# Optimization experiments

Hardware: AMD Instinct MI355X
Metric: run time of the kernel (lower is better)

Reference implementation:

```python
import jax, jax.numpy as jnp
import numpy as np

K = 4  # number of processing steps (init kwarg)


def setup_inputs() -> dict:
    key = jax.random.key(0)
    ks = jax.random.split(key, 6)
    B, S, D = 4096, 8192, 512
    H = D  # hidden_size == input_size (residual h + f_x)
    scale = 1.0 / np.sqrt(H)
    return {
        "f_x": jax.random.normal(ks[0], (B, D), dtype=jnp.float32),
        "g_S": jax.random.normal(ks[1], (S, D), dtype=jnp.float32),
        # LSTM step: input f_x (size D), 'hidden' is concat([h, r]) of size 2H
        "W_ih": jax.random.uniform(ks[2], (4 * H, D), jnp.float32, -scale, scale),
        "W_hh": jax.random.uniform(ks[3], (4 * H, 2 * H), jnp.float32, -scale, scale),
        "b_ih": jax.random.uniform(ks[4], (4 * H,), jnp.float32, -scale, scale),
        "b_hh": jax.random.uniform(ks[5], (4 * H,), jnp.float32, -scale, scale),
    }


def _lstm_step(x, hidden, c, W_ih, W_hh, b_ih, b_hh):
    # gates: [B, 4H]; PyTorch LSTMCell gate order (i, f, g, o)
    gates = x @ W_ih.T + b_ih + hidden @ W_hh.T + b_hh
    i, f, g, o = jnp.split(gates, 4, axis=1)
    c_new = jax.nn.sigmoid(f) * c + jax.nn.sigmoid(i) * jnp.tanh(g)
    h_new = jax.nn.sigmoid(o) * jnp.tanh(c_new)
    return h_new, c_new


def reference(f_x, g_S, W_ih, W_hh, b_ih, b_hh):
    # f_x: [B, D] queries; g_S: [S, D] support set embeddings
    h = f_x
    c = jnp.zeros_like(f_x)
    for _ in range(K):
        a = jax.nn.softmax(h @ g_S.T, axis=1)       # [B, S] attention over support
        r = a @ g_S                                  # [B, D] attention readout
        concat = jnp.concatenate([h, r], axis=1)     # [B, 2D]
        h, c = _lstm_step(f_x, concat, c, W_ih, W_hh, b_ih, b_hh)
        h = h + f_x                                  # residual skip connection
    return h
```

## Files before the change

### kernel.cpp

```cpp
#include <hip/hip_runtime.h>

typedef _Float16 f16x8 __attribute__((ext_vector_type(8)));
typedef _Float16 f16x4 __attribute__((ext_vector_type(4)));
typedef float f32x4 __attribute__((ext_vector_type(4)));

#define S_DIM 8192
#define D_DIM 512

__device__ __forceinline__ void gload_lds16(const _Float16* g, _Float16* l) {
  __builtin_amdgcn_global_load_lds(
      (const __attribute__((address_space(1))) unsigned int*)g,
      (__attribute__((address_space(3))) unsigned int*)l, 16, 0, 0);
}

__device__ __forceinline__ float sigf(float x) { return 1.0f / (1.0f + __expf(-x)); }
__device__ __forceinline__ float tanhfast(float x) {
  return 1.0f - 2.0f / (__expf(2.0f * x) + 1.0f);
}


template <int BM, int BN>
__global__ __launch_bounds__(256) void gemm_bt(const _Float16* __restrict__ A, int lda,
                                               const _Float16* __restrict__ B, int ldb,
                                               _Float16* __restrict__ C, int ldc, int K) {
  constexpr int BK = 64;
  constexpr int FM = BM / 32, FN = BN / 32;
  __shared__ _Float16 As[BM * BK];
  __shared__ _Float16 Bs[BN * BK];
  const int tid = threadIdx.x;
  const int lane = tid & 63;
  const int wv = tid >> 6;
  const int bm = blockIdx.y * BM;
  const int bn = blockIdx.x * BN;
  const int wm = (wv >> 1) * (BM / 2);
  const int wn = (wv & 1) * (BN / 2);
  const int fr = lane & 15;
  const int hi4 = lane >> 4;
  const int rx7 = fr & 7;
  const int srow = lane >> 3;
  const int schk = (lane & 7) ^ srow;

  f32x4 acc[FM][FN] = {};

  for (int kt = 0; kt < K; kt += BK) {
    __syncthreads();
#pragma unroll
    for (int p = 0; p < BM / 32; ++p) {
      const int m = wv + 4 * p;
      gload_lds16(A + (size_t)(bm + 8 * m + srow) * lda + kt + schk * 8, As + 512 * m);
    }
#pragma unroll
    for (int p = 0; p < BN / 32; ++p) {
      const int m = wv + 4 * p;
      gload_lds16(B + (size_t)(bn + 8 * m + srow) * ldb + kt + schk * 8, Bs + 512 * m);
    }
    __syncthreads();

#pragma unroll
    for (int h = 0; h < 2; ++h) {
      const int co = (((h << 2) | hi4) ^ rx7) << 3;
      f16x8 af[FM], bf[FN];
#pragma unroll
      for (int i = 0; i < FM; ++i)
        af[i] = *(const f16x8*)&As[(wm + i * 16 + fr) * 64 + co];
#pragma unroll
      for (int j = 0; j < FN; ++j)
        bf[j] = *(const f16x8*)&Bs[(wn + j * 16 + fr) * 64 + co];
#pragma unroll
      for (int i = 0; i < FM; ++i)
#pragma unroll
        for (int j = 0; j < FN; ++j)
          acc[i][j] = __builtin_amdgcn_mfma_f32_16x16x32_f16(af[i], bf[j], acc[i][j], 0, 0, 0);
    }
  }

  const int cc = lane & 15;
  const int cr = (lane >> 4) * 4;
#pragma unroll
  for (int i = 0; i < FM; ++i)
#pragma unroll
    for (int j = 0; j < FN; ++j) {
      size_t base = (size_t)(bm + wm + i * 16 + cr) * ldc + (bn + wn + j * 16 + cc);
#pragma unroll
      for (int r = 0; r < 4; ++r) C[base + (size_t)r * ldc] = (_Float16)acc[i][j][r];
    }
}

__global__ __launch_bounds__(256) void gemm_rsplit(const _Float16* __restrict__ A,
                                                   const _Float16* __restrict__ B,
                                                   float* __restrict__ Ppart) {
  constexpr int BK = 64;
  __shared__ _Float16 As[128 * BK];
  __shared__ _Float16 Bs[64 * BK];
  const int tid = threadIdx.x;
  const int lane = tid & 63;
  const int wv = tid >> 6;
  const int bm = blockIdx.x * 128;
  const int bn = blockIdx.y * 64;
  const int kc = blockIdx.z;
  const int k0 = kc * 1024;
  const int wm = (wv >> 1) * 64;
  const int wn = (wv & 1) * 32;
  const int fr = lane & 15;
  const int hi4 = lane >> 4;
  const int rx7 = fr & 7;
  const int srow = lane >> 3;
  const int schk = (lane & 7) ^ srow;

  f32x4 acc[4][2] = {};

  for (int kt = k0; kt < k0 + 1024; kt += BK) {
    __syncthreads();
#pragma unroll
    for (int p = 0; p < 4; ++p) {
      const int m = wv + 4 * p;
      gload_lds16(A + (size_t)(bm + 8 * m + srow) * 16384 + kt + schk * 8, As + 512 * m);
    }
#pragma unroll
    for (int p = 0; p < 2; ++p) {
      const int m = wv + 4 * p;
      gload_lds16(B + (size_t)(bn + 8 * m + srow) * 8192 + kt + schk * 8, Bs + 512 * m);
    }
    __syncthreads();

#pragma unroll
    for (int h = 0; h < 2; ++h) {
      const int co = (((h << 2) | hi4) ^ rx7) << 3;
      f16x8 af[4], bf[2];
#pragma unroll
      for (int i = 0; i < 4; ++i)
        af[i] = *(const f16x8*)&As[(wm + i * 16 + fr) * 64 + co];
#pragma unroll
      for (int j = 0; j < 2; ++j)
        bf[j] = *(const f16x8*)&Bs[(wn + j * 16 + fr) * 64 + co];
#pragma unroll
      for (int i = 0; i < 4; ++i)
#pragma unroll
        for (int j = 0; j < 2; ++j)
          acc[i][j] = __builtin_amdgcn_mfma_f32_16x16x32_f16(af[i], bf[j], acc[i][j], 0, 0, 0);
    }
  }

  const int cc = lane & 15;
  const int cr = (lane >> 4) * 4;
#pragma unroll
  for (int i = 0; i < 4; ++i)
#pragma unroll
    for (int j = 0; j < 2; ++j) {
      size_t base = (size_t)(bm + wm + i * 16 + cr) * 8192 + 4096 + (size_t)kc * 512 +
                    (bn + wn + j * 16 + cc);
#pragma unroll
      for (int r = 0; r < 4; ++r) Ppart[base + (size_t)r * 8192] = acc[i][j][r];
    }
}

__global__ __launch_bounds__(256) void reduce_r(const float* __restrict__ Ppart,
                                                _Float16* __restrict__ rout) {
  int idx = blockIdx.x * 256 + threadIdx.x;
  int m = idx >> 7;
  int n4 = (idx & 127) * 4;
  const float* base = Ppart + (size_t)m * 8192 + 4096 + n4;
  f32x4 s = {0.f, 0.f, 0.f, 0.f};
#pragma unroll
  for (int kc = 0; kc < 8; ++kc) s += *(const f32x4*)(base + kc * 512);
  f16x4 h = {(_Float16)s[0], (_Float16)s[1], (_Float16)s[2], (_Float16)s[3]};
  *(f16x4*)&rout[(size_t)m * 512 + n4] = h;
}

__global__ __launch_bounds__(256) void gemm_scores(const _Float16* __restrict__ Ah, int ldah,
                                                   const _Float16* __restrict__ Al,
                                                   const _Float16* __restrict__ Bh,
                                                   float* __restrict__ C) {
  constexpr int BK = 64;
  __shared__ _Float16 AsH[128 * BK];
  __shared__ _Float16 AsL[128 * BK];
  __shared__ _Float16 BsH[128 * BK];
  const int tid = threadIdx.x;
  const int lane = tid & 63;
  const int wv = tid >> 6;
  const int bm = blockIdx.y * 128;
  const int bn = blockIdx.x * 128;
  const int wm = (wv >> 1) * 64;
  const int wn = (wv & 1) * 64;
  const int fr = lane & 15;
  const int hi4 = lane >> 4;
  const int rx7 = fr & 7;
  const int srow = lane >> 3;
  const int schk = (lane & 7) ^ srow;

  f32x4 acc[4][4] = {};

  for (int kt = 0; kt < 512; kt += BK) {
    __syncthreads();
#pragma unroll
    for (int p = 0; p < 4; ++p) {
      const int m = wv + 4 * p;
      const int row = 8 * m + srow;
      gload_lds16(Ah + (size_t)(bm + row) * ldah + kt + schk * 8, AsH + 512 * m);
      gload_lds16(Al + (size_t)(bm + row) * 512 + kt + schk * 8, AsL + 512 * m);
      gload_lds16(Bh + (size_t)(bn + row) * 512 + kt + schk * 8, BsH + 512 * m);
    }
    __syncthreads();

#pragma unroll
    for (int h = 0; h < 2; ++h) {
      const int co = (((h << 2) | hi4) ^ rx7) << 3;
      f16x8 fah[4], fal[4], fbh[4];
#pragma unroll
      for (int i = 0; i < 4; ++i) {
        fah[i] = *(const f16x8*)&AsH[(wm + i * 16 + fr) * 64 + co];
        fal[i] = *(const f16x8*)&AsL[(wm + i * 16 + fr) * 64 + co];
        fbh[i] = *(const f16x8*)&BsH[(wn + i * 16 + fr) * 64 + co];
      }
#pragma unroll
      for (int i = 0; i < 4; ++i)
#pragma unroll
        for (int j = 0; j < 4; ++j) {
          acc[i][j] = __builtin_amdgcn_mfma_f32_16x16x32_f16(fah[i], fbh[j], acc[i][j], 0, 0, 0);
          acc[i][j] = __builtin_amdgcn_mfma_f32_16x16x32_f16(fal[i], fbh[j], acc[i][j], 0, 0, 0);
        }
    }
  }

  const int cc = lane & 15;
  const int cr = (lane >> 4) * 4;
#pragma unroll
  for (int i = 0; i < 4; ++i)
#pragma unroll
    for (int j = 0; j < 4; ++j) {
      size_t base = (size_t)(bm + wm + i * 16 + cr) * 8192 + (bn + wn + j * 16 + cc);
#pragma unroll
      for (int r = 0; r < 4; ++r) C[base + (size_t)r * 8192] = acc[i][j][r];
    }
}

__global__ __launch_bounds__(256) void gemm_gates(const _Float16* __restrict__ Ah,
                                                  const _Float16* __restrict__ Ar,
                                                  const _Float16* __restrict__ B,
                                                  const _Float16* __restrict__ gbase,
                                                  const float* __restrict__ bsum,
                                                  const float* __restrict__ f_x,
                                                  float* __restrict__ c,
                                                  _Float16* __restrict__ hnext,
                                                  _Float16* __restrict__ h_lo,
                                                  float* __restrict__ hout) {
  __shared__ _Float16 As[128 * 64];
  __shared__ _Float16 Bs[128 * 64];
  const int tid = threadIdx.x;
  const int lane = tid & 63;
  const int wv = tid >> 6;
  const int n0 = blockIdx.x * 32;
  const int bm = blockIdx.y * 128;
  const int fr = lane & 15;
  const int hi4 = lane >> 4;
  const int rx7 = fr & 7;
  const int srow = lane >> 3;
  const int schk = (lane & 7) ^ srow;

  f32x4 acc[2][8] = {};

  for (int t = 0; t < 16; ++t) {
    const int kt = t * 64;
    __syncthreads();
#pragma unroll
    for (int p = 0; p < 4; ++p) {
      const int m = wv + 4 * p;
      const int arow = bm + 8 * m + srow;
      const _Float16* asrc = (t < 8)
                                 ? Ah + (size_t)arow * 512 + kt + schk * 8
                                 : Ar + (size_t)arow * 512 + (kt - 512) + schk * 8;
      gload_lds16(asrc, As + 512 * m);
      const int brow = 8 * m + srow;
      const int wrow = ((brow >> 5) << 9) + n0 + (brow & 31);
      gload_lds16(B + (size_t)wrow * 1024 + kt + schk * 8, Bs + 512 * m);
    }
    __syncthreads();

#pragma unroll
    for (int h = 0; h < 2; ++h) {
      const int co = (((h << 2) | hi4) ^ rx7) << 3;
      f16x8 af[2], bf[8];
#pragma unroll
      for (int i = 0; i < 2; ++i)
        af[i] = *(const f16x8*)&As[(wv * 32 + i * 16 + fr) * 64 + co];
#pragma unroll
      for (int j = 0; j < 8; ++j)
        bf[j] = *(const f16x8*)&Bs[(j * 16 + fr) * 64 + co];
#pragma unroll
      for (int i = 0; i < 2; ++i)
#pragma unroll
        for (int j = 0; j < 8; ++j)
          acc[i][j] = __builtin_amdgcn_mfma_f32_16x16x32_f16(af[i], bf[j], acc[i][j], 0, 0, 0);
    }
  }

  const int cc = lane & 15;
  const int cr = (lane >> 4) * 4;
#pragma unroll
  for (int jj = 0; jj < 2; ++jj) {
    const int colq = n0 + jj * 16 + cc;
    const float bI = bsum[colq];
    const float bF = bsum[colq + 512];
    const float bG = bsum[colq + 1024];
    const float bO = bsum[colq + 1536];
#pragma unroll
    for (int i = 0; i < 2; ++i)
#pragma unroll
      for (int r = 0; r < 4; ++r) {
        const int row = bm + wv * 32 + i * 16 + cr + r;
        const size_t g0 = (size_t)row * 2048 + colq;
        const float gi = acc[i][jj][r] + (float)gbase[g0] + bI;
        const float gf = acc[i][2 + jj][r] + (float)gbase[g0 + 512] + bF;
        const float gg = acc[i][4 + jj][r] + (float)gbase[g0 + 1024] + bG;
        const float go = acc[i][6 + jj][r] + (float)gbase[g0 + 1536] + bO;
        const size_t o = (size_t)row * 512 + colq;
        const float ci = sigf(gf) * c[o] + sigf(gi) * tanhfast(gg);
        const float hi = sigf(go) * tanhfast(ci) + f_x[o];
        c[o] = ci;
        hout[o] = hi;
        const _Float16 h16 = (_Float16)hi;
        hnext[o] = h16;
        h_lo[o] = (_Float16)(hi - (float)h16);
      }
  }
}

__global__ __launch_bounds__(256) void prep_g(const float* __restrict__ g,
                                              _Float16* __restrict__ gT,
                                              _Float16* __restrict__ g_h) {
  __shared__ _Float16 tile[64][72];
  const int s0 = blockIdx.x * 64;
  const int d0 = blockIdx.y * 64;
  const int t = threadIdx.x;
  const int r = t >> 2;
  const int cq = (t & 3) * 16;
  alignas(16) _Float16 buf[16];
#pragma unroll
  for (int q = 0; q < 4; ++q) {
    f32x4 v = *(const f32x4*)&g[(size_t)(s0 + r) * D_DIM + d0 + cq + q * 4];
#pragma unroll
    for (int e = 0; e < 4; ++e) buf[q * 4 + e] = (_Float16)v[e];
  }
#pragma unroll
  for (int k = 0; k < 16; ++k) tile[r][cq + k] = buf[k];
  *(f16x8*)&g_h[(size_t)(s0 + r) * D_DIM + d0 + cq] = *(const f16x8*)&buf[0];
  *(f16x8*)&g_h[(size_t)(s0 + r) * D_DIM + d0 + cq + 8] = *(const f16x8*)&buf[8];
  __syncthreads();
  alignas(16) _Float16 ob[16];
#pragma unroll
  for (int k = 0; k < 16; ++k) ob[k] = tile[cq + k][r];
  *(f16x8*)&gT[(size_t)(d0 + r) * S_DIM + s0 + cq] = *(const f16x8*)&ob[0];
  *(f16x8*)&gT[(size_t)(d0 + r) * S_DIM + s0 + cq + 8] = *(const f16x8*)&ob[8];
}

__global__ __launch_bounds__(256) void prep_misc(const float* __restrict__ W_ih,
                                                 const float* __restrict__ W_hh,
                                                 const float* __restrict__ f_x,
                                                 const float* __restrict__ b_ih,
                                                 const float* __restrict__ b_hh,
                                                 _Float16* __restrict__ wih_h,
                                                 _Float16* __restrict__ whh_h,
                                                 _Float16* __restrict__ hbufA,
                                                 _Float16* __restrict__ h_lo,
                                                 float* __restrict__ c,
                                                 float* __restrict__ bsum) {
  const int NW1 = 2048 * 512 / 4;
  const int NW2 = 2048 * 1024 / 4;
  const int NFX = 4096 * 512 / 4;
  int idx = blockIdx.x * 256 + threadIdx.x;
  if (idx < NW1) {
    f32x4 v = ((const f32x4*)W_ih)[idx];
    f16x4 h = {(_Float16)v[0], (_Float16)v[1], (_Float16)v[2], (_Float16)v[3]};
    ((f16x4*)wih_h)[idx] = h;
  } else if (idx < NW1 + NW2) {
    int k = idx - NW1;
    f32x4 v = ((const f32x4*)W_hh)[k];
    f16x4 h = {(_Float16)v[0], (_Float16)v[1], (_Float16)v[2], (_Float16)v[3]};
    ((f16x4*)whh_h)[k] = h;
  } else if (idx < NW1 + NW2 + NFX) {
    int k = idx - NW1 - NW2;
    f32x4 v = ((const f32x4*)f_x)[k];
    f16x4 h, lo;
#pragma unroll
    for (int e = 0; e < 4; ++e) {
      h[e] = (_Float16)v[e];
      lo[e] = (_Float16)(v[e] - (float)h[e]);
    }
    ((f16x4*)hbufA)[k] = h;
    ((f16x4*)h_lo)[k] = lo;
    f32x4 z = {0.f, 0.f, 0.f, 0.f};
    ((f32x4*)c)[k] = z;
  } else if (idx < NW1 + NW2 + NFX + 512) {
    int k = idx - NW1 - NW2 - NFX;
    f32x4 bi = ((const f32x4*)b_ih)[k];
    f32x4 bh = ((const f32x4*)b_hh)[k];
    ((f32x4*)bsum)[k] = bi + bh;
  }
}

__global__ __launch_bounds__(256) void softmax_inplace(float* __restrict__ P) {
  float* p = P + (size_t)blockIdx.x * S_DIM;
  const int tid = threadIdx.x, lane = tid & 63, wave = tid >> 6;
  __shared__ float red[8];
  float x[32];
#pragma unroll
  for (int i = 0; i < 8; ++i) {
    f32x4 v = *(const f32x4*)&p[i * 1024 + tid * 4];
#pragma unroll
    for (int j = 0; j < 4; ++j) x[i * 4 + j] = v[j];
  }
  float m = -3.0e38f;
#pragma unroll
  for (int k = 0; k < 32; ++k) m = fmaxf(m, x[k]);
#pragma unroll
  for (int o = 32; o; o >>= 1) m = fmaxf(m, __shfl_xor(m, o));
  if (lane == 0) red[wave] = m;
  __syncthreads();
  m = fmaxf(fmaxf(red[0], red[1]), fmaxf(red[2], red[3]));
  float s = 0.f;
#pragma unroll
  for (int k = 0; k < 32; ++k) {
    x[k] = exp2f((x[k] - m) * 1.44269504f);
    s += x[k];
  }
#pragma unroll
  for (int o = 32; o; o >>= 1) s += __shfl_xor(s, o);
  if (lane == 0) red[4 + wave] = s;
  __syncthreads();
  s = (red[4] + red[5]) + (red[6] + red[7]);
  float inv = 1.0f / s;
  _Float16* out = (_Float16*)p;
#pragma unroll
  for (int i = 0; i < 8; ++i) {
    f16x4 v;
#pragma unroll
    for (int j = 0; j < 4; ++j) v[j] = (_Float16)(x[i * 4 + j] * inv);
    *(f16x4*)&out[i * 1024 + tid * 4] = v;
  }
}

extern "C" void kernel_launch(void* const* d_in, const int* in_sizes, int n_in,
                              void* d_out, int out_size, void* d_ws, size_t ws_size,
                              hipStream_t stream) {
  const float* f_x = (const float*)d_in[0];
  const float* g_S = (const float*)d_in[1];
  const float* W_ih = (const float*)d_in[2];
  const float* W_hh = (const float*)d_in[3];
  const float* b_ih = (const float*)d_in[4];
  const float* b_hh = (const float*)d_in[5];
  float* hout = (float*)d_out;

  char* w = (char*)d_ws;
  float* P32 = (float*)w;
  _Float16* gbase = (_Float16*)(w + 67108864);
  _Float16* hbufA = (_Float16*)(w + 83886080);
  _Float16* hbufB = (_Float16*)(w + 88080384);
  _Float16* g_h = (_Float16*)(w + 92274688);
  _Float16* rbuf = (_Float16*)(w + 100663296);
  float* bsum = (float*)(w + 104857600);
  _Float16* gT = (_Float16*)(w + 109051904);
  _Float16* wih_h = (_Float16*)(w + 117440512);
  _Float16* whh_h = (_Float16*)(w + 119537664);
  float* c = (float*)(w + 123731968);
  _Float16* h_lo = (_Float16*)(w + 132120576);

  prep_g<<<dim3(S_DIM / 64, D_DIM / 64), 256, 0, stream>>>(g_S, gT, g_h);
  prep_misc<<<5122, 256, 0, stream>>>(W_ih, W_hh, f_x, b_ih, b_hh, wih_h, whh_h,
                                      hbufA, h_lo, c, bsum);

  gemm_bt<128, 128><<<dim3(2048 / 128, 4096 / 128), 256, 0, stream>>>(
      hbufA, 512, wih_h, 512, gbase, 2048, 512);

  for (int it = 0; it < 4; ++it) {
    _Float16* hcur = (it & 1) ? hbufB : hbufA;
    _Float16* hnxt = (it & 1) ? hbufA : hbufB;
    for (int hb = 0; hb < 2; ++hb) {
      const _Float16* hhi = hcur + (size_t)hb * 2048 * 512;
      const _Float16* hlo = h_lo + (size_t)hb * 2048 * 512;
      gemm_scores<<<dim3(64, 16), 256, 0, stream>>>(hhi, 512, hlo, g_h, P32);
      softmax_inplace<<<2048, 256, 0, stream>>>(P32);
      gemm_rsplit<<<dim3(16, 8, 8), 256, 0, stream>>>((const _Float16*)P32, gT, P32);
      reduce_r<<<1024, 256, 0, stream>>>(P32, rbuf + (size_t)hb * 2048 * 512);
    }
    gemm_gates<<<dim3(16, 32), 256, 0, stream>>>(hcur, rbuf, whh_h, gbase, bsum,
                                                 f_x, c, hnxt, h_lo, hout);
  }
  (void)in_sizes; (void)n_in; (void)out_size; (void)ws_size;
}
```

Baseline: 855.7 us.

## Fuse per-tile row max into score GEMM and store scores as fp16

The score GEMM now reduces a per-row max within each 128-column tile, writes tile-relative scores (score minus tile max) as fp16, and writes the tile maxima to a small buffer. A new softmax kernel combines those tile maxima into the global row max and rescales, so it reads fp16 instead of fp32 and no longer needs a max-reduction pass. The split-K partials for the readout GEMM are also stored in fp16 in a separate buffer rather than fp32. Together this roughly halves the memory traffic for the score matrix and the partials. The cost is lost precision in the fp16 relative scores and in the fp16 partial sums.

Measured after the change: 866.6 us. No clear change (+1.3%).

```diff
diff --git a/kernel.cpp b/kernel.cpp
--- a/kernel.cpp
+++ b/kernel.cpp
@@ -88,7 +88,7 @@
 
 __global__ __launch_bounds__(256) void gemm_rsplit(const _Float16* __restrict__ A,
                                                    const _Float16* __restrict__ B,
-                                                   float* __restrict__ Ppart) {
+                                                   _Float16* __restrict__ Pp) {
   constexpr int BK = 64;
   __shared__ _Float16 As[128 * BK];
   __shared__ _Float16 Bs[64 * BK];
@@ -114,7 +114,7 @@
 #pragma unroll
     for (int p = 0; p < 4; ++p) {
       const int m = wv + 4 * p;
-      gload_lds16(A + (size_t)(bm + 8 * m + srow) * 16384 + kt + schk * 8, As + 512 * m);
+      gload_lds16(A + (size_t)(bm + 8 * m + srow) * 8192 + kt + schk * 8, As + 512 * m);
     }
 #pragma unroll
     for (int p = 0; p < 2; ++p) {
@@ -147,34 +147,41 @@
   for (int i = 0; i < 4; ++i)
 #pragma unroll
     for (int j = 0; j < 2; ++j) {
-      size_t base = (size_t)(bm + wm + i * 16 + cr) * 8192 + 4096 + (size_t)kc * 512 +
+      size_t base = (size_t)(bm + wm + i * 16 + cr) * 4096 + (size_t)kc * 512 +
                     (bn + wn + j * 16 + cc);
 #pragma unroll
-      for (int r = 0; r < 4; ++r) Ppart[base + (size_t)r * 8192] = acc[i][j][r];
-    }
-}
-
-__global__ __launch_bounds__(256) void reduce_r(const float* __restrict__ Ppart,
+      for (int r = 0; r < 4; ++r) Pp[base + (size_t)r * 4096] = (_Float16)acc[i][j][r];
+    }
+}
+
+__global__ __launch_bounds__(256) void reduce_r(const _Float16* __restrict__ Pp,
                                                 _Float16* __restrict__ rout) {
   int idx = blockIdx.x * 256 + threadIdx.x;
   int m = idx >> 7;
   int n4 = (idx & 127) * 4;
-  const float* base = Ppart + (size_t)m * 8192 + 4096 + n4;
+  const _Float16* base = Pp + (size_t)m * 4096 + n4;
   f32x4 s = {0.f, 0.f, 0.f, 0.f};
 #pragma unroll
-  for (int kc = 0; kc < 8; ++kc) s += *(const f32x4*)(base + kc * 512);
+  for (int kc = 0; kc < 8; ++kc) {
+    f16x4 v = *(const f16x4*)(base + kc * 512);
+#pragma unroll
+    for (int e = 0; e < 4; ++e) s[e] += (float)v[e];
+  }
   f16x4 h = {(_Float16)s[0], (_Float16)s[1], (_Float16)s[2], (_Float16)s[3]};
   *(f16x4*)&rout[(size_t)m * 512 + n4] = h;
 }
 
-__global__ __launch_bounds__(256) void gemm_scores(const _Float16* __restrict__ Ah, int ldah,
-                                                   const _Float16* __restrict__ Al,
-                                                   const _Float16* __restrict__ Bh,
-                                                   float* __restrict__ C) {
+__global__ __launch_bounds__(256) void gemm_scores_rel(const _Float16* __restrict__ Ah,
+                                                       int ldah,
+                                                       const _Float16* __restrict__ Al,
+                                                       const _Float16* __restrict__ Bh,
+                                                       _Float16* __restrict__ P,
+                                                       float* __restrict__ M) {
   constexpr int BK = 64;
   __shared__ _Float16 AsH[128 * BK];
   __shared__ _Float16 AsL[128 * BK];
   __shared__ _Float16 BsH[128 * BK];
+  __shared__ float rm[2][128];
   const int tid = threadIdx.x;
   const int lane = tid & 63;
   const int wv = tid >> 6;
@@ -224,14 +231,78 @@
 
   const int cc = lane & 15;
   const int cr = (lane >> 4) * 4;
+  float rmax[4][4];
 #pragma unroll
   for (int i = 0; i < 4; ++i)
 #pragma unroll
-    for (int j = 0; j < 4; ++j) {
-      size_t base = (size_t)(bm + wm + i * 16 + cr) * 8192 + (bn + wn + j * 16 + cc);
-#pragma unroll
-      for (int r = 0; r < 4; ++r) C[base + (size_t)r * 8192] = acc[i][j][r];
-    }
+    for (int r = 0; r < 4; ++r) {
+      float m0 = fmaxf(fmaxf(acc[i][0][r], acc[i][1][r]),
+                       fmaxf(acc[i][2][r], acc[i][3][r]));
+#pragma unroll
+      for (int o = 1; o < 16; o <<= 1) m0 = fmaxf(m0, __shfl_xor(m0, o));
+      rmax[i][r] = m0;
+    }
+  if (cc == 0) {
+#pragma unroll
+    for (int i = 0; i < 4; ++i)
+#pragma unroll
+      for (int r = 0; r < 4; ++r) rm[wv & 1][wm + i * 16 + cr + r] = rmax[i][r];
+  }
+  __syncthreads();
+#pragma unroll
+  for (int i = 0; i < 4; ++i)
+#pragma unroll
+    for (int r = 0; r < 4; ++r) {
+      const int row = wm + i * 16 + cr + r;
+      const float mt = fmaxf(rm[0][row], rm[1][row]);
+      if (cc == 0 && (wv & 1) == 0)
+        M[(size_t)(bm + row) * 64 + blockIdx.x] = mt;
+#pragma unroll
+      for (int j = 0; j < 4; ++j)
+        P[(size_t)(bm + row) * 8192 + bn + wn + j * 16 + cc] =
+            (_Float16)(acc[i][j][r] - mt);
+    }
+}
+
+__global__ __launch_bounds__(256) void softmax2(_Float16* __restrict__ P,
+                                                const float* __restrict__ M) {
+  _Float16* p = P + (size_t)blockIdx.x * S_DIM;
+  const float* Mr = M + (size_t)blockIdx.x * 64;
+  const int tid = threadIdx.x, lane = tid & 63, wave = tid >> 6;
+  __shared__ float red[4];
+  __shared__ float mt[64];
+  if (tid < 64) mt[tid] = Mr[tid];
+  __syncthreads();
+  float mstar = -3.0e38f;
+#pragma unroll 8
+  for (int j = 0; j < 64; ++j) mstar = fmaxf(mstar, mt[j]);
+  float x[32];
+#pragma unroll
+  for (int i = 0; i < 4; ++i) {
+    f16x8 v = *(const f16x8*)&p[i * 2048 + tid * 8];
+    const float off = mt[i * 16 + (tid >> 4)] - mstar;
+#pragma unroll
+    for (int j = 0; j < 8; ++j) x[i * 8 + j] = (float)v[j] + off;
+  }
+  float s = 0.f;
+#pragma unroll
+  for (int k = 0; k < 32; ++k) {
+    x[k] = exp2f(x[k] * 1.44269504f);
+    s += x[k];
+  }
+#pragma unroll
+  for (int o = 32; o; o >>= 1) s += __shfl_xor(s, o);
+  if (lane == 0) red[wave] = s;
+  __syncthreads();
+  s = (red[0] + red[1]) + (red[2] + red[3]);
+  float inv = 1.0f / s;
+#pragma unroll
+  for (int i = 0; i < 4; ++i) {
+    f16x8 v;
+#pragma unroll
+    for (int j = 0; j < 8; ++j) v[j] = (_Float16)(x[i * 8 + j] * inv);
+    *(f16x8*)&p[i * 2048 + tid * 8] = v;
+  }
 }
 
 __global__ __launch_bounds__(256) void gemm_gates(const _Float16* __restrict__ Ah,
@@ -398,47 +469,6 @@
   }
 }
 
-__global__ __launch_bounds__(256) void softmax_inplace(float* __restrict__ P) {
-  float* p = P + (size_t)blockIdx.x * S_DIM;
-  const int tid = threadIdx.x, lane = tid & 63, wave = tid >> 6;
-  __shared__ float red[8];
-  float x[32];
-#pragma unroll
-  for (int i = 0; i < 8; ++i) {
-    f32x4 v = *(const f32x4*)&p[i * 1024 + tid * 4];
-#pragma unroll
-    for (int j = 0; j < 4; ++j) x[i * 4 + j] = v[j];
-  }
-  float m = -3.0e38f;
-#pragma unroll
-  for (int k = 0; k < 32; ++k) m = fmaxf(m, x[k]);
-#pragma unroll
-  for (int o = 32; o; o >>= 1) m = fmaxf(m, __shfl_xor(m, o));
-  if (lane == 0) red[wave] = m;
-  __syncthreads();
-  m = fmaxf(fmaxf(red[0], red[1]), fmaxf(red[2], red[3]));
-  float s = 0.f;
-#pragma unroll
-  for (int k = 0; k < 32; ++k) {
-    x[k] = exp2f((x[k] - m) * 1.44269504f);
-    s += x[k];
-  }
-#pragma unroll
-  for (int o = 32; o; o >>= 1) s += __shfl_xor(s, o);
-  if (lane == 0) red[4 + wave] = s;
-  __syncthreads();
-  s = (red[4] + red[5]) + (red[6] + red[7]);
-  float inv = 1.0f / s;
-  _Float16* out = (_Float16*)p;
-#pragma unroll
-  for (int i = 0; i < 8; ++i) {
-    f16x4 v;
-#pragma unroll
-    for (int j = 0; j < 4; ++j) v[j] = (_Float16)(x[i * 4 + j] * inv);
-    *(f16x4*)&out[i * 1024 + tid * 4] = v;
-  }
-}
-
 extern "C" void kernel_launch(void* const* d_in, const int* in_sizes, int n_in,
                               void* d_out, int out_size, void* d_ws, size_t ws_size,
                               hipStream_t stream) {
@@ -451,7 +481,9 @@
   float* hout = (float*)d_out;
 
   char* w = (char*)d_ws;
-  float* P32 = (float*)w;
+  _Float16* P16 = (_Float16*)w;
+  _Float16* Pp16 = (_Float16*)(w + 33554432);
+  float* Mbuf = (float*)(w + 50331648);
   _Float16* gbase = (_Float16*)(w + 67108864);
   _Float16* hbufA = (_Float16*)(w + 83886080);
   _Float16* hbufB = (_Float16*)(w + 88080384);
@@ -477,10 +509,10 @@
     for (int hb = 0; hb < 2; ++hb) {
       const _Float16* hhi = hcur + (size_t)hb * 2048 * 512;
       const _Float16* hlo = h_lo + (size_t)hb * 2048 * 512;
-      gemm_scores<<<dim3(64, 16), 256, 0, stream>>>(hhi, 512, hlo, g_h, P32);
-      softmax_inplace<<<2048, 256, 0, stream>>>(P32);
-      gemm_rsplit<<<dim3(16, 8, 8), 256, 0, stream>>>((const _Float16*)P32, gT, P32);
-      reduce_r<<<1024, 256, 0, stream>>>(P32, rbuf + (size_t)hb * 2048 * 512);
+      gemm_scores_rel<<<dim3(64, 16), 256, 0, stream>>>(hhi, 512, hlo, g_h, P16, Mbuf);
+      softmax2<<<2048, 256, 0, stream>>>(P16, Mbuf);
+      gemm_rsplit<<<dim3(16, 8, 8), 256, 0, stream>>>(P16, gT, Pp16);
+      reduce_r<<<1024, 256, 0, stream>>>(Pp16, rbuf + (size_t)hb * 2048 * 512);
     }
     gemm_gates<<<dim3(16, 32), 256, 0, stream>>>(hcur, rbuf, whh_h, gbase, bsum,
                                                  f_x, c, hnxt, h_lo, hout);
```
